# Kernel optimization log

Hardware: AMD Instinct MI355X
Metric: run time of the kernel (lower is better)

The kernel has to match this reference:

```python
import jax, jax.numpy as jnp
import numpy as np

B, N, C_IN, D, K = 4, 512, 256, 256, 20


def setup_inputs() -> dict:
    key = jax.random.key(0)
    ks = jax.random.split(key, 6)
    s_in = 1.0 / np.sqrt(C_IN)
    return {
        "x": jax.random.normal(ks[0], (B, N, C_IN), dtype=jnp.float32),
        "edge_index": jnp.zeros((2, 4), dtype=jnp.int64),
        "batch": jnp.zeros((B * N,), dtype=jnp.int64),
        "W_l": jax.random.uniform(ks[1], (D, C_IN), jnp.float32, -s_in, s_in),
        "b_l": jax.random.uniform(ks[2], (D,), jnp.float32, -s_in, s_in),
        "W_r": jax.random.uniform(ks[3], (D, C_IN), jnp.float32, -s_in, s_in),
        "b_r": jax.random.uniform(ks[4], (D,), jnp.float32, -s_in, s_in),
        "att": jax.random.normal(ks[5], (1, D), dtype=jnp.float32) * 0.1,
    }


def reference(x, edge_index, batch, W_l, b_l, W_r, b_r, att):
    b, n, _ = x.shape
    k = K
    # linear projections -> [b, n, d]
    x_l = jnp.einsum("bnc,dc->bnd", x, W_l) + b_l
    x_r = jnp.einsum("bnc,dc->bnd", x, W_r) + b_r
    # pairwise additive attention: [b, n, n, d]
    pair = x_l[:, :, None, :] + x_r[:, None, :, :]
    pair = jnp.where(pair >= 0, pair, 0.2 * pair)  # leaky_relu(0.2)
    alpha = jnp.einsum("bijd,d->bij", pair, att[0])  # [b, n, n]
    alpha = jnp.nan_to_num(alpha, nan=0.0, posinf=0.0, neginf=0.0)
    # knn reduction: topk over last dim
    attention, indices = jax.lax.top_k(alpha, k)  # [b, n, k]
    attention = jax.nn.softmax(attention, axis=-1).reshape(-1)  # [b*n*k]
    # edge index construction with per-batch node offsets
    offset = (jnp.arange(b, dtype=indices.dtype) * n)[:, None]  # [b, 1]
    index_i = jnp.repeat(jnp.arange(n, dtype=indices.dtype), k)[None, :] + offset
    index_j = indices.reshape(b, n * k) + offset
    new_edge_index = jnp.stack([index_i.reshape(-1), index_j.reshape(-1)], axis=0)
    # dropout is identity in eval mode; learn_sys=False -> return directly
    return new_edge_index, attention
```

## Files before the change

kernel.cpp:

```cpp
#include <hip/hip_runtime.h>
#include <math.h>


#define GLD_LDS(gp, lp)                                                        \
    __builtin_amdgcn_global_load_lds(                                          \
        (const __attribute__((address_space(1))) float*)(gp),                  \
        (__attribute__((address_space(3))) float*)(lp), 16, 0, 0)

__global__ __launch_bounds__(256) void k_uv(const float* __restrict__ Wl,
        const float* __restrict__ Wr, const float* __restrict__ bl,
        const float* __restrict__ br, const float* __restrict__ att,
        float* __restrict__ ul, float* __restrict__ ur, float* __restrict__ cs) {
    __shared__ float red[4];
    const int g = blockIdx.x, tid = threadIdx.x;
    float p;
    if (g < 512) {
        const int side = g >> 8, c = g & 255;
        const float* W = side ? Wr : Wl;
        p = att[tid] * W[(size_t)tid * 256 + c];
    } else {
        const float* bb = (g == 512) ? bl : br;
        p = att[tid] * bb[tid];
    }
#pragma unroll
    for (int off = 32; off; off >>= 1) p += __shfl_xor(p, off);
    if ((tid & 63) == 0) red[tid >> 6] = p;
    __syncthreads();
    if (tid == 0) {
        const float s = red[0] + red[1] + red[2] + red[3];
        if (g < 256) ul[g] = s;
        else if (g < 512) ur[g - 256] = s;
        else cs[g - 512] = s;
    }
}

__global__ __launch_bounds__(256) void k_transpose(const float* __restrict__ x,
        const float* __restrict__ Wl, const float* __restrict__ Wr,
        const float* __restrict__ ul, const float* __restrict__ ur,
        const float* __restrict__ cs,
        float* __restrict__ WtL, float* __restrict__ WtR, float* __restrict__ xT,
        float* __restrict__ Av, float* __restrict__ Bv) {
    __shared__ float red[8];
    const int g = blockIdx.x, c = threadIdx.x;
    if (g < 256)      { WtL[c * 256 + g] = Wl[g * 256 + c]; return; }
    else if (g < 512) { WtR[c * 256 + (g - 256)] = Wr[(g - 256) * 256 + c]; return; }
    const int r = g - 512;
    const float xv = x[(size_t)r * 256 + c];
    xT[(size_t)c * 2048 + r] = xv;
    float p = xv * ul[c];
    float q = xv * ur[c];
#pragma unroll
    for (int off = 32; off; off >>= 1) {
        p += __shfl_xor(p, off);
        q += __shfl_xor(q, off);
    }
    if ((c & 63) == 0) { red[c >> 6] = p; red[4 + (c >> 6)] = q; }
    __syncthreads();
    if (c == 0) Av[r] = red[0] + red[1] + red[2] + red[3] + cs[0];
    if (c == 1) Bv[r] = red[4] + red[5] + red[6] + red[7] + cs[1];
}

__global__ __launch_bounds__(256, 1) void k_proj(const float* __restrict__ xT,
        const float* __restrict__ WtL, const float* __restrict__ WtR,
        const float* __restrict__ bl, const float* __restrict__ br,
        float* __restrict__ XL, float* __restrict__ XRt) {
    __shared__ __align__(16) float xst[256 * 64];
    __shared__ __align__(16) float wst[256 * 64];
    const int tid = threadIdx.x;
    const int lane = tid & 63;
    const int wv = tid >> 6;
    const int g = blockIdx.x;
    const int side = g & 1;
    const int dq = (g >> 1) & 3;
    const int rb = g >> 3;
    const int R = rb * 64;
    const int d0 = dq * 64;
    const int b = R >> 9;
    const float* __restrict__ W = side ? WtR : WtL;

#pragma unroll
    for (int n = 0; n < 16; ++n) {
        const int f4 = (n * 4 + wv) * 64 + lane;
        const int c = f4 >> 4, k4 = f4 & 15;
        GLD_LDS(xT + (size_t)c * 2048 + R + k4 * 4, &xst[(n * 4 + wv) * 256]);
        GLD_LDS(W + (size_t)c * 256 + d0 + k4 * 4, &wst[(n * 4 + wv) * 256]);
    }
    __syncthreads();

    const int rt = tid & 15;
    const int dt = tid >> 4;
    float acc[4][4];
#pragma unroll
    for (int r = 0; r < 4; ++r)
#pragma unroll
        for (int k = 0; k < 4; ++k) acc[r][k] = 0.f;

    const float* xp = &xst[rt * 4];
    const float* wp = &wst[dt * 4];
#pragma unroll 8
    for (int c = 0; c < 256; ++c) {
        const float4 xv = *(const float4*)(xp + c * 64);
        const float4 wq = *(const float4*)(wp + c * 64);
#define PROJ_R(r, XS)                              \
        acc[r][0] = fmaf(XS, wq.x, acc[r][0]);     \
        acc[r][1] = fmaf(XS, wq.y, acc[r][1]);     \
        acc[r][2] = fmaf(XS, wq.z, acc[r][2]);     \
        acc[r][3] = fmaf(XS, wq.w, acc[r][3]);
        PROJ_R(0, xv.x)
        PROJ_R(1, xv.y)
        PROJ_R(2, xv.z)
        PROJ_R(3, xv.w)
#undef PROJ_R
    }

    const float4 bias = *(const float4*)&(side ? br : bl)[d0 + dt * 4];
    if (side == 0) {
#pragma unroll
        for (int r = 0; r < 4; ++r) {
            *(float4*)&XL[(size_t)(R + rt * 4 + r) * 256 + d0 + dt * 4] =
                make_float4(acc[r][0] + bias.x, acc[r][1] + bias.y,
                            acc[r][2] + bias.z, acc[r][3] + bias.w);
        }
    } else {
        const int jr = (R & 511) + rt * 4;
#pragma unroll
        for (int k = 0; k < 4; ++k) {
            const int d = d0 + dt * 4 + k;
            const float bk = k == 0 ? bias.x : k == 1 ? bias.y : k == 2 ? bias.z : bias.w;
            *(float4*)&XRt[((size_t)(b * 256 + d)) * 512 + jr] =
                make_float4(acc[0][k] + bk, acc[1][k] + bk,
                            acc[2][k] + bk, acc[3][k] + bk);
        }
    }
}

__global__ __launch_bounds__(512, 2) void k_pair_topk(const float* __restrict__ XL,
        const float* __restrict__ XRt, const float* __restrict__ Av,
        const float* __restrict__ Bv, const float* __restrict__ att,
        float* __restrict__ out) {
    __shared__ __align__(16) float xls[8 * 256];
    __shared__ __align__(16) float atts[256];
    __shared__ __align__(16) float mrg[3 * 4096];
    __shared__ __align__(16) float alph[8 * 512];
    const int tid = threadIdx.x;
    const int jc = tid & 127;
    const int h = tid >> 7;
    const int g = blockIdx.x;
    const int R = g * 8, b = R >> 9;

    ((float4*)xls)[tid] = ((const float4*)(XL + (size_t)R * 256))[tid];
    if (tid < 64) ((float4*)atts)[tid] = ((const float4*)att)[tid];
    __syncthreads();

    const int dbase = h * 64;
    const float* __restrict__ xrp = XRt + (size_t)b * 131072 + (size_t)dbase * 512 + jc * 4;

    float acc[8][4];
#pragma unroll
    for (int i = 0; i < 8; ++i)
#pragma unroll
        for (int c = 0; c < 4; ++c) acc[i][c] = 0.f;

    float4 bufA[8], bufB[8];
#pragma unroll
    for (int dd = 0; dd < 8; ++dd) bufA[dd] = *(const float4*)(xrp + (size_t)dd * 512);

#pragma unroll
    for (int ch = 0; ch < 8; ++ch) {
        const float4* cur = (ch & 1) ? bufB : bufA;
        float4* nxt = (ch & 1) ? bufA : bufB;
        if (ch < 7) {
            const float* p = xrp + (size_t)(ch + 1) * 8 * 512;
#pragma unroll
            for (int dd = 0; dd < 8; ++dd) nxt[dd] = *(const float4*)(p + (size_t)dd * 512);
        }
        const int d0 = dbase + ch * 8;
        const float4 at0 = *(const float4*)&atts[d0];
        const float4 at1 = *(const float4*)&atts[d0 + 4];
#pragma unroll
        for (int i = 0; i < 8; ++i) {
            const float4 xa = *(const float4*)&xls[i * 256 + d0];
            const float4 xb = *(const float4*)&xls[i * 256 + d0 + 4];
#define PSTEP(XLC, ATC, XR4)                                       \
            acc[i][0] = fmaf(ATC, fabsf(XLC + XR4.x), acc[i][0]);   \
            acc[i][1] = fmaf(ATC, fabsf(XLC + XR4.y), acc[i][1]);   \
            acc[i][2] = fmaf(ATC, fabsf(XLC + XR4.z), acc[i][2]);   \
            acc[i][3] = fmaf(ATC, fabsf(XLC + XR4.w), acc[i][3]);
            PSTEP(xa.x, at0.x, cur[0])
            PSTEP(xa.y, at0.y, cur[1])
            PSTEP(xa.z, at0.z, cur[2])
            PSTEP(xa.w, at0.w, cur[3])
            PSTEP(xb.x, at1.x, cur[4])
            PSTEP(xb.y, at1.y, cur[5])
            PSTEP(xb.z, at1.z, cur[6])
            PSTEP(xb.w, at1.w, cur[7])
#undef PSTEP
        }
    }

    if (h) {
        float* m = &mrg[(h - 1) * 4096];
#pragma unroll
        for (int i = 0; i < 8; ++i)
            *(float4*)&m[i * 512 + jc * 4] =
                make_float4(acc[i][0], acc[i][1], acc[i][2], acc[i][3]);
    }
    __syncthreads();
    if (h == 0) {
        const float4 Bj = *(const float4*)&Bv[b * 512 + jc * 4];
#pragma unroll
        for (int i = 0; i < 8; ++i) {
            const float Ai = Av[R + i];
            const float4 m0 = *(const float4*)&mrg[i * 512 + jc * 4];
            const float4 m1 = *(const float4*)&mrg[4096 + i * 512 + jc * 4];
            const float4 m2 = *(const float4*)&mrg[8192 + i * 512 + jc * 4];
            float a0 = fmaf(0.4f, acc[i][0] + m0.x + m1.x + m2.x, 0.6f * (Ai + Bj.x));
            float a1 = fmaf(0.4f, acc[i][1] + m0.y + m1.y + m2.y, 0.6f * (Ai + Bj.y));
            float a2 = fmaf(0.4f, acc[i][2] + m0.z + m1.z + m2.z, 0.6f * (Ai + Bj.z));
            float a3 = fmaf(0.4f, acc[i][3] + m0.w + m1.w + m2.w, 0.6f * (Ai + Bj.w));
            if (!isfinite(a0)) a0 = 0.f;
            if (!isfinite(a1)) a1 = 0.f;
            if (!isfinite(a2)) a2 = 0.f;
            if (!isfinite(a3)) a3 = 0.f;
            *(float4*)&alph[i * 512 + jc * 4] = make_float4(a0, a1, a2, a3);
        }
    }
    __syncthreads();

    const int lane = tid & 63;
    const int i = tid >> 6;
    const float* ar = &alph[i * 512];
    const float4 u0 = *(const float4*)&ar[lane * 8];
    const float4 u1 = *(const float4*)&ar[lane * 8 + 4];
    float v[8] = {u0.x, u0.y, u0.z, u0.w, u1.x, u1.y, u1.z, u1.w};

    float myval = 0.f, mmax = 0.f;
    int myidx = 0;
    for (int sel = 0; sel < 20; ++sel) {
        float bv = v[0]; int bt = 0;
#pragma unroll
        for (int t = 1; t < 8; ++t) { if (v[t] > bv) { bv = v[t]; bt = t; } }
        int bj = lane * 8 + bt;
#pragma unroll
        for (int off = 32; off; off >>= 1) {
            const float ov = __shfl_xor(bv, off);
            const int   oj = __shfl_xor(bj, off);
            if (ov > bv || (ov == bv && oj < bj)) { bv = ov; bj = oj; }
        }
        if (sel == 0) mmax = bv;
        if (lane == sel) { myval = bv; myidx = bj; }
        if ((bj >> 3) == lane) {
            const int bt2 = bj & 7;
#pragma unroll
            for (int t = 0; t < 8; ++t) if (t == bt2) v[t] = -INFINITY;
        }
    }
    const float e = (lane < 20) ? expf(myval - mmax) : 0.f;
    float s = e;
#pragma unroll
    for (int off = 32; off; off >>= 1) s += __shfl_xor(s, off);
    if (lane < 20) {
        const int row = R + i;
        const int base = row * 20 + lane;
        out[base] = (float)row;
        out[40960 + base] = (float)(b * 512 + myidx);
        out[81920 + base] = e / s;
    }
}

extern "C" void kernel_launch(void* const* d_in, const int* in_sizes, int n_in,
                              void* d_out, int out_size, void* d_ws, size_t ws_size,
                              hipStream_t stream) {
    const float* x   = (const float*)d_in[0];
    const float* Wl  = (const float*)d_in[3];
    const float* bl  = (const float*)d_in[4];
    const float* Wr  = (const float*)d_in[5];
    const float* br  = (const float*)d_in[6];
    const float* att = (const float*)d_in[7];

    float* ws  = (float*)d_ws;
    float* WtL = ws;
    float* WtR = ws + 65536;
    float* xT  = ws + 131072;
    float* XL  = ws + 1048576;
    float* XRt = ws + 1572864;
    float* Av  = ws + 2097152;
    float* Bv  = ws + 2099200;
    float* ul  = ws + 2101248;
    float* ur  = ws + 2101504;
    float* cs  = ws + 2101760;
    float* out = (float*)d_out;

    k_uv<<<dim3(514), dim3(256), 0, stream>>>(Wl, Wr, bl, br, att, ul, ur, cs);
    k_transpose<<<dim3(2560), dim3(256), 0, stream>>>(x, Wl, Wr, ul, ur, cs,
                                                      WtL, WtR, xT, Av, Bv);
    k_proj<<<dim3(256), dim3(256), 0, stream>>>(xT, WtL, WtR, bl, br, XL, XRt);
    k_pair_topk<<<dim3(256), dim3(512), 0, stream>>>(XL, XRt, Av, Bv, att, out);
}
```

Baseline: 128.5 us.

## Restructure projection GEMM with split-K across waves and smaller row tiles

The projection kernel moves from 64-row by 64-col tiles with full LDS staging via global_load_lds to 16-row tiles with 512 threads. The reduction dimension is split four ways across thread groups, and partial sums are merged through LDS. Weights are read straight from global memory into registers, and the left and right projections are computed together in one block. This is meant to raise occupancy and block count (512 blocks instead of 256), at the cost of redundant weight reads per block, an extra LDS reduction step, and scalar strided stores to XRt.

```diff
diff --git a/kernel.cpp b/kernel.cpp
--- a/kernel.cpp
+++ b/kernel.cpp
@@ -1,11 +1,6 @@
 #include <hip/hip_runtime.h>
 #include <math.h>
 
-
-#define GLD_LDS(gp, lp)                                                        \
-    __builtin_amdgcn_global_load_lds(                                          \
-        (const __attribute__((address_space(1))) float*)(gp),                  \
-        (__attribute__((address_space(3))) float*)(lp), 16, 0, 0)
 
 __global__ __launch_bounds__(256) void k_uv(const float* __restrict__ Wl,
         const float* __restrict__ Wr, const float* __restrict__ bl,
@@ -60,76 +55,110 @@
     if (c == 1) Bv[r] = red[4] + red[5] + red[6] + red[7] + cs[1];
 }
 
-__global__ __launch_bounds__(256, 1) void k_proj(const float* __restrict__ xT,
+__global__ __launch_bounds__(512, 2) void k_proj(const float* __restrict__ xT,
         const float* __restrict__ WtL, const float* __restrict__ WtR,
         const float* __restrict__ bl, const float* __restrict__ br,
         float* __restrict__ XL, float* __restrict__ XRt) {
-    __shared__ __align__(16) float xst[256 * 64];
-    __shared__ __align__(16) float wst[256 * 64];
+    __shared__ __align__(16) float xst[256 * 16];
+    __shared__ __align__(16) float mrg[3 * 2048];
     const int tid = threadIdx.x;
-    const int lane = tid & 63;
-    const int wv = tid >> 6;
     const int g = blockIdx.x;
-    const int side = g & 1;
-    const int dq = (g >> 1) & 3;
-    const int rb = g >> 3;
-    const int R = rb * 64;
-    const int d0 = dq * 64;
+    const int db = g & 3;
+    const int rb = g >> 2;
+    const int R = rb * 16, d0 = db * 64;
     const int b = R >> 9;
-    const float* __restrict__ W = side ? WtR : WtL;
-
-#pragma unroll
-    for (int n = 0; n < 16; ++n) {
-        const int f4 = (n * 4 + wv) * 64 + lane;
-        const int c = f4 >> 4, k4 = f4 & 15;
-        GLD_LDS(xT + (size_t)c * 2048 + R + k4 * 4, &xst[(n * 4 + wv) * 256]);
-        GLD_LDS(W + (size_t)c * 256 + d0 + k4 * 4, &wst[(n * 4 + wv) * 256]);
-    }
-    __syncthreads();
-
-    const int rt = tid & 15;
-    const int dt = tid >> 4;
-    float acc[4][4];
-#pragma unroll
-    for (int r = 0; r < 4; ++r)
-#pragma unroll
-        for (int k = 0; k < 4; ++k) acc[r][k] = 0.f;
-
-    const float* xp = &xst[rt * 4];
-    const float* wp = &wst[dt * 4];
-#pragma unroll 8
-    for (int c = 0; c < 256; ++c) {
-        const float4 xv = *(const float4*)(xp + c * 64);
-        const float4 wq = *(const float4*)(wp + c * 64);
-#define PROJ_R(r, XS)                              \
-        acc[r][0] = fmaf(XS, wq.x, acc[r][0]);     \
-        acc[r][1] = fmaf(XS, wq.y, acc[r][1]);     \
-        acc[r][2] = fmaf(XS, wq.z, acc[r][2]);     \
-        acc[r][3] = fmaf(XS, wq.w, acc[r][3]);
-        PROJ_R(0, xv.x)
-        PROJ_R(1, xv.y)
-        PROJ_R(2, xv.z)
-        PROJ_R(3, xv.w)
-#undef PROJ_R
-    }
-
-    const float4 bias = *(const float4*)&(side ? br : bl)[d0 + dt * 4];
-    if (side == 0) {
-#pragma unroll
-        for (int r = 0; r < 4; ++r) {
-            *(float4*)&XL[(size_t)(R + rt * 4 + r) * 256 + d0 + dt * 4] =
-                make_float4(acc[r][0] + bias.x, acc[r][1] + bias.y,
-                            acc[r][2] + bias.z, acc[r][3] + bias.w);
-        }
-    } else {
-        const int jr = (R & 511) + rt * 4;
+    const int ch = tid >> 7;
+    const int rg = (tid >> 4) & 7;
+    const int dq = tid & 15;
+
+    for (int s = tid; s < 1024; s += 512) {
+        const int c = s >> 2, q = s & 3;
+        *(float4*)&xst[c * 16 + q * 4] =
+            *(const float4*)&xT[(size_t)c * 2048 + R + q * 4];
+    }
+    __syncthreads();
+
+    float accL[2][4], accR[2][4];
+#pragma unroll
+    for (int rr = 0; rr < 2; ++rr)
+#pragma unroll
+        for (int k = 0; k < 4; ++k) { accL[rr][k] = 0.f; accR[rr][k] = 0.f; }
+
+    const int c0 = ch * 64;
+    const float* WLp = WtL + (size_t)c0 * 256 + d0 + dq * 4;
+    const float* WRp = WtR + (size_t)c0 * 256 + d0 + dq * 4;
+
+#pragma unroll 2
+    for (int cb = 0; cb < 16; ++cb) {
+        float4 wl[4], wr[4];
 #pragma unroll
         for (int k = 0; k < 4; ++k) {
-            const int d = d0 + dt * 4 + k;
-            const float bk = k == 0 ? bias.x : k == 1 ? bias.y : k == 2 ? bias.z : bias.w;
-            *(float4*)&XRt[((size_t)(b * 256 + d)) * 512 + jr] =
-                make_float4(acc[0][k] + bk, acc[1][k] + bk,
-                            acc[2][k] + bk, acc[3][k] + bk);
+            wl[k] = *(const float4*)(WLp + (size_t)(cb * 4 + k) * 256);
+            wr[k] = *(const float4*)(WRp + (size_t)(cb * 4 + k) * 256);
+        }
+#pragma unroll
+        for (int k = 0; k < 4; ++k) {
+            const float2 xv = *(const float2*)&xst[(c0 + cb * 4 + k) * 16 + rg * 2];
+            accL[0][0] = fmaf(xv.x, wl[k].x, accL[0][0]);
+            accL[0][1] = fmaf(xv.x, wl[k].y, accL[0][1]);
+            accL[0][2] = fmaf(xv.x, wl[k].z, accL[0][2]);
+            accL[0][3] = fmaf(xv.x, wl[k].w, accL[0][3]);
+            accL[1][0] = fmaf(xv.y, wl[k].x, accL[1][0]);
+            accL[1][1] = fmaf(xv.y, wl[k].y, accL[1][1]);
+            accL[1][2] = fmaf(xv.y, wl[k].z, accL[1][2]);
+            accL[1][3] = fmaf(xv.y, wl[k].w, accL[1][3]);
+            accR[0][0] = fmaf(xv.x, wr[k].x, accR[0][0]);
+            accR[0][1] = fmaf(xv.x, wr[k].y, accR[0][1]);
+            accR[0][2] = fmaf(xv.x, wr[k].z, accR[0][2]);
+            accR[0][3] = fmaf(xv.x, wr[k].w, accR[0][3]);
+            accR[1][0] = fmaf(xv.y, wr[k].x, accR[1][0]);
+            accR[1][1] = fmaf(xv.y, wr[k].y, accR[1][1]);
+            accR[1][2] = fmaf(xv.y, wr[k].z, accR[1][2]);
+            accR[1][3] = fmaf(xv.y, wr[k].w, accR[1][3]);
+        }
+    }
+
+    if (ch > 0) {
+        float* m = &mrg[(ch - 1) * 2048];
+#pragma unroll
+        for (int rr = 0; rr < 2; ++rr) {
+            const int base = (rg * 2 + rr) * 128;
+            *(float4*)&m[base + dq * 4] =
+                make_float4(accL[rr][0], accL[rr][1], accL[rr][2], accL[rr][3]);
+            *(float4*)&m[base + 64 + dq * 4] =
+                make_float4(accR[rr][0], accR[rr][1], accR[rr][2], accR[rr][3]);
+        }
+    }
+    __syncthreads();
+
+    if (ch == 0) {
+        const float4 blv = *(const float4*)&bl[d0 + dq * 4];
+        const float4 brv = *(const float4*)&br[d0 + dq * 4];
+#pragma unroll
+        for (int rr = 0; rr < 2; ++rr) {
+            const int base = (rg * 2 + rr) * 128 + dq * 4;
+            const float4 l0 = *(const float4*)&mrg[base];
+            const float4 l1 = *(const float4*)&mrg[2048 + base];
+            const float4 l2 = *(const float4*)&mrg[4096 + base];
+            const float4 r0 = *(const float4*)&mrg[base + 64];
+            const float4 r1 = *(const float4*)&mrg[2048 + base + 64];
+            const float4 r2 = *(const float4*)&mrg[4096 + base + 64];
+            float sl[4], sr[4];
+            sl[0] = accL[rr][0] + l0.x + l1.x + l2.x + blv.x;
+            sl[1] = accL[rr][1] + l0.y + l1.y + l2.y + blv.y;
+            sl[2] = accL[rr][2] + l0.z + l1.z + l2.z + blv.z;
+            sl[3] = accL[rr][3] + l0.w + l1.w + l2.w + blv.w;
+            sr[0] = accR[rr][0] + r0.x + r1.x + r2.x + brv.x;
+            sr[1] = accR[rr][1] + r0.y + r1.y + r2.y + brv.y;
+            sr[2] = accR[rr][2] + r0.z + r1.z + r2.z + brv.z;
+            sr[3] = accR[rr][3] + r0.w + r1.w + r2.w + brv.w;
+            const int row = R + rg * 2 + rr;
+            *(float4*)&XL[(size_t)row * 256 + d0 + dq * 4] =
+                make_float4(sl[0], sl[1], sl[2], sl[3]);
+            const int j = (row & 511);
+#pragma unroll
+            for (int k = 0; k < 4; ++k)
+                XRt[((size_t)(b * 256 + d0 + dq * 4 + k)) * 512 + j] = sr[k];
         }
     }
 }
@@ -294,6 +323,6 @@
     k_uv<<<dim3(514), dim3(256), 0, stream>>>(Wl, Wr, bl, br, att, ul, ur, cs);
     k_transpose<<<dim3(2560), dim3(256), 0, stream>>>(x, Wl, Wr, ul, ur, cs,
                                                       WtL, WtR, xT, Av, Bv);
-    k_proj<<<dim3(256), dim3(256), 0, stream>>>(xT, WtL, WtR, bl, br, XL, XRt);
+    k_proj<<<dim3(512), dim3(512), 0, stream>>>(xT, WtL, WtR, bl, br, XL, XRt);
     k_pair_topk<<<dim3(256), dim3(512), 0, stream>>>(XL, XRt, Av, Bv, att, out);
 }
```

New measurement: 135.3 us. 1.05x slower.
